# Performance work log

Measured on AMD Instinct MI355X. Metric: run time of the kernel, lower is better.

The kernel has to match this reference:

```python
import jax, jax.numpy as jnp
import numpy as np

DIM = 1024
HEAD_SIZE = 128
B, N = 4, 4096

def setup_inputs() -> dict:
    key = jax.random.key(0)
    kx, kq, kk, kv = jax.random.split(key, 4)
    s = (1.0 / DIM) ** 0.5  # ~ torch Linear init scale
    return {
        "x": jax.random.normal(kx, (B, N, DIM), dtype=jnp.float32),
        "Wq": jax.random.uniform(kq, (HEAD_SIZE, DIM), dtype=jnp.float32, minval=-s, maxval=s),
        "Wk": jax.random.uniform(kk, (HEAD_SIZE, DIM), dtype=jnp.float32, minval=-s, maxval=s),
        "Wv": jax.random.uniform(kv, (HEAD_SIZE, DIM), dtype=jnp.float32, minval=-s, maxval=s),
    }

def reference(x, Wq, Wk, Wv):
    # x: [B, N, dim]; W*: [head_size, dim] (torch Linear convention y = x @ W.T)
    q = jnp.einsum('bnd,hd->bnh', x, Wq)
    k = jnp.einsum('bnd,hd->bnh', x, Wk)
    v = jnp.einsum('bnd,hd->bnh', x, Wv)
    scale = DIM ** (-0.5)  # NOTE: original scales by dim**-0.5, not head_size
    scores = jnp.einsum('bnh,bmh->bnm', q, k) * scale  # [B, N, N]
    weights = jax.nn.softmax(scores, axis=-1)
    context = jnp.einsum('bnm,bmh->bnh', weights, v)  # [B, N, head_size]
    return context
```

## Files before the change

kernel.cpp:

```cpp
#include <hip/hip_runtime.h>

using bf16x8   = __attribute__((ext_vector_type(8))) __bf16;
using f32x4    = __attribute__((ext_vector_type(4))) float;
using f32x16   = __attribute__((ext_vector_type(16))) float;
using floatv4  = __attribute__((ext_vector_type(4))) float;
using ushortv4 = __attribute__((ext_vector_type(4))) unsigned short;
using ushortv8 = __attribute__((ext_vector_type(8))) unsigned short;
using uintv2   = __attribute__((ext_vector_type(2))) unsigned int;
using uintv4   = __attribute__((ext_vector_type(4))) unsigned int;

#define N_SEQ 4096
#define N_B   4
#define DIMK  1024
#define HS    128
#define ROWS  (N_B * N_SEQ)
#define KVB   32
#define TT    (N_SEQ / KVB)
#define CEXPF 0.045084220027780106f

__device__ __forceinline__ unsigned short f2bf(float f) {
    unsigned u = __builtin_bit_cast(unsigned, f);
    u += 0x7FFFu + ((u >> 16) & 1u);
    return (unsigned short)(u >> 16);
}

__device__ __forceinline__ unsigned cvtpk(float lo, float hi) {
    unsigned r;
    asm("v_cvt_pk_bf16_f32 %0, %1, %2" : "=v"(r) : "v"(lo), "v"(hi));
    return r;
}

__device__ __forceinline__ void gload16(const unsigned short* g, unsigned short* l) {
    __builtin_amdgcn_global_load_lds(
        (const __attribute__((address_space(1))) unsigned int*)g,
        (__attribute__((address_space(3))) unsigned int*)l, 16, 0, 0);
}

__global__ __launch_bounds__(256) void castw_kernel(
    const float* __restrict__ Wq,
    const float* __restrict__ Wk,
    const float* __restrict__ Wv,
    unsigned short* __restrict__ Wb2)
{
    const int blk = blockIdx.x;
    const int z = blk >> 6;
    const int b2 = blk & 63;
    const float* src = (z == 0) ? Wq : (z == 1) ? Wk : Wv;
    const float scale = (z == 0) ? CEXPF : 1.0f;

    const int oo = b2 * 256 + threadIdx.x;
    const int slot = oo & 3;
    const int row  = (oo >> 2) & 127;
    const int ks   = oo >> 9;
    const int slog = (slot - (row >> 1)) & 3;
    const int k0   = ks * 32 + slog * 8;

    floatv4 a = *reinterpret_cast<const floatv4*>(src + (size_t)row * DIMK + k0);
    floatv4 b = *reinterpret_cast<const floatv4*>(src + (size_t)row * DIMK + k0 + 4);
    ushortv8 o = { f2bf(a.x*scale), f2bf(a.y*scale), f2bf(a.z*scale), f2bf(a.w*scale),
                   f2bf(b.x*scale), f2bf(b.y*scale), f2bf(b.z*scale), f2bf(b.w*scale) };
    unsigned short* dst = Wb2 + (size_t)ks * 12288 + (size_t)z * 4096 + ((row * 4 + slot) * 8);
    *reinterpret_cast<ushortv8*>(dst) = o;
}

__global__ __launch_bounds__(512, 1) void proj_kernel(
    const float* __restrict__ X,
    const unsigned short* __restrict__ Wb2,
    unsigned short* __restrict__ Qb,
    unsigned short* __restrict__ Kb,
    unsigned short* __restrict__ Vt)
{
    const int row0 = blockIdx.x * 64;
    __shared__ unsigned short smem[2 * 64 * 40 + 2 * 384 * 32];
    unsigned short* Xs = smem;
    unsigned short* Ws = smem + 2 * 64 * 40;
    const int tid = threadIdx.x;
    const int wv = tid >> 6, lane = tid & 63;
    const int lr = lane & 15, lg = lane >> 4;

    const int xr_r = tid >> 3, xr_q = tid & 7;
    const float* xgbase = X + (size_t)(row0 + xr_r) * DIMK + xr_q * 4;

    f32x4 acc[4][3] = {};

    auto loadX = [&](floatv4& xr, int ks) {
        xr = *reinterpret_cast<const floatv4*>(xgbase + ks * 32);
    };
    auto writeX = [&](int buf, const floatv4& xr) {
        uintv2 w = { cvtpk(xr.x, xr.y), cvtpk(xr.z, xr.w) };
        *reinterpret_cast<uintv2*>(&Xs[buf * (64 * 40) + xr_r * 40 + xr_q * 4]) = w;
    };
    auto stageW = [&](int buf, int ks) {
        const unsigned short* src = Wb2 + (size_t)ks * 12288;
        unsigned short* dst = Ws + buf * 12288;
        #pragma unroll
        for (int jj = 0; jj < 3; ++jj)
            gload16(src + (size_t)(jj * 512 + wv * 64 + lane) * 8,
                    dst + (jj * 512 + wv * 64) * 8);
    };

    int zni[3], wrow0[3];
    #pragma unroll
    for (int ni = 0; ni < 3; ++ni) {
        int gc0 = wv * 48 + ni * 16;
        zni[ni] = gc0 >> 7;
        wrow0[ni] = gc0 & 127;
    }

    floatv4 xrA, xrB;
    loadX(xrB, 0); stageW(0, 0);
    loadX(xrA, 1); stageW(1, 1);
    asm volatile("s_waitcnt vmcnt(4)" ::: "memory");
    writeX(0, xrB);
    __syncthreads();

#define PROJ_ITER(KS, XN, XM, CUR)                                             \
    {                                                                          \
        const unsigned short* Xc = Xs + (CUR) * (64 * 40);                     \
        const unsigned short* Wc = Ws + (CUR) * 12288;                         \
        bf16x8 af[4]; bf16x8 bfr[3];                                           \
        _Pragma("unroll")                                                      \
        for (int mi = 0; mi < 4; ++mi)                                         \
            af[mi] = *reinterpret_cast<const bf16x8*>(                         \
                &Xc[(mi * 16 + lr) * 40 + lg * 8]);                            \
        _Pragma("unroll")                                                      \
        for (int ni = 0; ni < 3; ++ni) {                                       \
            int wrow = wrow0[ni] + lr;                                         \
            bfr[ni] = *reinterpret_cast<const bf16x8*>(                        \
                &Wc[((zni[ni] * 128 + wrow) * 4 + ((lg + (wrow >> 1)) & 3)) * 8]); \
        }                                                                      \
        _Pragma("unroll")                                                      \
        for (int mi = 0; mi < 4; ++mi)                                         \
            _Pragma("unroll")                                                  \
            for (int ni = 0; ni < 3; ++ni)                                     \
                acc[mi][ni] = __builtin_amdgcn_mfma_f32_16x16x32_bf16(         \
                    af[mi], bfr[ni], acc[mi][ni], 0, 0, 0);                    \
        __syncthreads();                                                       \
        if ((KS) + 2 < 32) { loadX(XM, (KS) + 2); stageW((CUR), (KS) + 2); }   \
        if ((KS) + 1 < 32) {                                                   \
            if ((KS) + 2 < 32)                                                 \
                asm volatile("s_waitcnt vmcnt(4)" ::: "memory");               \
            else                                                               \
                asm volatile("s_waitcnt vmcnt(0)" ::: "memory");               \
            writeX((CUR) ^ 1, XN);                                             \
            __syncthreads();                                                   \
        }                                                                      \
    }

    for (int kss = 0; kss < 32; kss += 2) {
        PROJ_ITER(kss,     xrA, xrB, 0);
        PROJ_ITER(kss + 1, xrB, xrA, 1);
    }
#undef PROJ_ITER

    unsigned short* Cs = smem;
    #pragma unroll
    for (int ni = 0; ni < 3; ++ni) {
        const int z = zni[ni];
        if (z < 2) {
            unsigned short* O = (z == 0) ? Qb : Kb;
            const int col = wrow0[ni] + lr;
            #pragma unroll
            for (int mi = 0; mi < 4; ++mi) {
                int rowb = row0 + mi * 16 + lg * 4;
                #pragma unroll
                for (int r = 0; r < 4; ++r)
                    O[(size_t)(rowb + r) * HS + col] = f2bf(acc[mi][ni][r]);
            }
        } else {
            const int col = wrow0[ni] + lr;
            #pragma unroll
            for (int mi = 0; mi < 4; ++mi)
                #pragma unroll
                for (int r = 0; r < 4; ++r)
                    Cs[(mi * 16 + lg * 4 + r) * 136 + col] = f2bf(acc[mi][ni][r]);
        }
    }
    __syncthreads();
    {
        const int b  = row0 >> 12;
        const int n0 = row0 & (N_SEQ - 1);
        #pragma unroll
        for (int i = 0; i < 2; ++i) {
            int idx = tid + i * 512;
            int d = idx >> 3, c8 = idx & 7;
            ushortv8 v;
            #pragma unroll
            for (int j = 0; j < 8; ++j)
                v[j] = Cs[(c8 * 8 + j) * 136 + d];
            *reinterpret_cast<ushortv8*>(Vt + (size_t)b * HS * N_SEQ + (size_t)d * N_SEQ + n0 + c8 * 8) = v;
        }
    }
}

__global__ __launch_bounds__(256, 3) void attn_kernel(
    const unsigned short* __restrict__ Qb,
    const unsigned short* __restrict__ Kb,
    const unsigned short* __restrict__ Vt,
    unsigned short* __restrict__ part,
    float* __restrict__ plsum,
    int S)
{
    const int qblk  = blockIdx.x;
    const int split = blockIdx.y;
    const int tid = threadIdx.x;
    const int wv = tid >> 6, lane = tid & 63;
    const int l31 = lane & 31, h = lane >> 5;
    const int b    = qblk >> 5;
    const int row0 = (qblk & 31) * 128 + wv * 32;

    __shared__ unsigned short Ks[3][KVB * 128];
    __shared__ unsigned short Vs[3][128 * KVB];

    bf16x8 qf[8];
    {
        const unsigned short* qp = Qb + ((size_t)b * N_SEQ + row0 + l31) * HS + h * 8;
        #pragma unroll
        for (int kk = 0; kk < 8; ++kk)
            qf[kk] = *reinterpret_cast<const bf16x8*>(qp + kk * 16);
    }

    const int base = TT / S, rem = TT % S;
    const int nt = base + (split < rem ? 1 : 0);
    const int kv_begin = (split * base + (split < rem ? split : rem)) * KVB;

    const unsigned short* Kbb = Kb + (size_t)b * N_SEQ * HS;
    const unsigned short* Vbb = Vt + (size_t)b * HS * N_SEQ;

    auto stage = [&](int buf, int kv0) {
        #pragma unroll
        for (int i = 0; i < 2; ++i) {
            int g = wv * 2 + i;
            int r = g * 4 + (lane >> 4);
            int sp = (lane & 15) ^ (r & 7);
            gload16(Kbb + (size_t)(kv0 + r) * HS + sp * 8, &Ks[buf][g * 4 * 128]);
        }
        #pragma unroll
        for (int i = 0; i < 2; ++i) {
            int g = wv * 2 + i;
            int r = g * 16 + (lane >> 2);
            int sp = (lane & 3) ^ ((r >> 1) & 3);
            gload16(Vbb + (size_t)r * N_SEQ + kv0 + sp * 8, &Vs[buf][g * 16 * KVB]);
        }
    };

    f32x16 ctx[4] = {};
    float lsum = 0.f;

    stage(0, kv_begin);
    stage(1, kv_begin + KVB);
    int cur = 0, nxt = 2;
    for (int t = 0; t < nt; ++t) {
        if (t + 2 < nt) {
            asm volatile("s_waitcnt vmcnt(4)\n\ts_barrier" ::: "memory");
            stage(nxt, kv_begin + (t + 2) * KVB);
        } else if (t + 1 < nt) {
            asm volatile("s_waitcnt vmcnt(4)\n\ts_barrier" ::: "memory");
        } else {
            asm volatile("s_waitcnt vmcnt(0)\n\ts_barrier" ::: "memory");
        }

        f32x16 st0 = {}, st1 = {};
        __builtin_amdgcn_s_setprio(1);
        #pragma unroll
        for (int kk = 0; kk < 8; kk += 2) {
            bf16x8 kf0 = *reinterpret_cast<const bf16x8*>(
                &Ks[cur][l31 * 128 + (((kk * 2 + h) ^ (l31 & 7)) * 8)]);
            st0 = __builtin_amdgcn_mfma_f32_32x32x16_bf16(kf0, qf[kk], st0, 0, 0, 0);
            bf16x8 kf1 = *reinterpret_cast<const bf16x8*>(
                &Ks[cur][l31 * 128 + ((((kk + 1) * 2 + h) ^ (l31 & 7)) * 8)]);
            st1 = __builtin_amdgcn_mfma_f32_32x32x16_bf16(kf1, qf[kk + 1], st1, 0, 0, 0);
        }
        __builtin_amdgcn_s_setprio(0);

        float p[16];
        #pragma unroll
        for (int r = 0; r < 16; ++r)
            p[r] = __builtin_amdgcn_exp2f(st0[r] + st1[r]);

        {
            float a0 = (p[0] + p[1])   + (p[2] + p[3]);
            float a1 = (p[4] + p[5])   + (p[6] + p[7]);
            float a2 = (p[8] + p[9])   + (p[10] + p[11]);
            float a3 = (p[12] + p[13]) + (p[14] + p[15]);
            lsum += (a0 + a1) + (a2 + a3);
        }

        bf16x8 pf[2];
        #pragma unroll
        for (int half = 0; half < 2; ++half) {
            unsigned a  = cvtpk(p[half*8 + 0], p[half*8 + 1]);
            unsigned bq = cvtpk(p[half*8 + 2], p[half*8 + 3]);
            unsigned c  = cvtpk(p[half*8 + 4], p[half*8 + 5]);
            unsigned d  = cvtpk(p[half*8 + 6], p[half*8 + 7]);
            asm("v_permlane32_swap_b32 %0, %1" : "+v"(a), "+v"(c));
            asm("v_permlane32_swap_b32 %0, %1" : "+v"(bq), "+v"(d));
            uintv4 w = { a, bq, c, d };
            pf[half] = __builtin_bit_cast(bf16x8, w);
        }

        __builtin_amdgcn_s_setprio(1);
        #pragma unroll
        for (int dt = 0; dt < 4; ++dt) {
            int d = dt * 32 + l31;
            bf16x8 vf0 = *reinterpret_cast<const bf16x8*>(
                &Vs[cur][d * KVB + (((0 + h) ^ ((d >> 1) & 3)) * 8)]);
            ctx[dt] = __builtin_amdgcn_mfma_f32_32x32x16_bf16(pf[0], vf0, ctx[dt], 0, 0, 0);
            bf16x8 vf1 = *reinterpret_cast<const bf16x8*>(
                &Vs[cur][d * KVB + (((2 + h) ^ ((d >> 1) & 3)) * 8)]);
            ctx[dt] = __builtin_amdgcn_mfma_f32_32x32x16_bf16(pf[1], vf1, ctx[dt], 0, 0, 0);
        }
        __builtin_amdgcn_s_setprio(0);

        cur = (cur == 2) ? 0 : cur + 1;
        nxt = (nxt == 2) ? 0 : nxt + 1;
    }

    lsum += __shfl_xor(lsum, 32);

    const int qt = qblk * 4 + wv;
    unsigned short* pp = part + ((size_t)qt * S + split) * (32 * 128);
    #pragma unroll
    for (int rp = 0; rp < 4; ++rp)
        #pragma unroll
        for (int rq = 0; rq < 4; ++rq) {
            const int r = rp * 4 + rq;
            const int q = rq + 8 * rp + 4 * h;
            #pragma unroll
            for (int dt = 0; dt < 4; ++dt)
                pp[q * 128 + dt * 32 + l31] = (unsigned short)(cvtpk(ctx[dt][r], ctx[dt][r]) & 0xFFFFu);
        }
    if (h == 0)
        plsum[((size_t)qt * S + split) * 32 + l31] = lsum;
}

__global__ __launch_bounds__(256) void reduce_kernel(
    const unsigned short* __restrict__ part,
    const float* __restrict__ plsum,
    float* __restrict__ out, int S)
{
    const int id = blockIdx.x * 256 + threadIdx.x;
    const int d4 = (id & 31) * 4;
    const int grow = id >> 5;
    const int qt = grow >> 5, q = grow & 31;
    f32x4 c = {0.f, 0.f, 0.f, 0.f};
    float l = 0.f;
    for (int s = 0; s < S; ++s) {
        ushortv4 pv = *reinterpret_cast<const ushortv4*>(
            &part[(((size_t)qt * S + s) * 32 + q) * 128 + d4]);
        #pragma unroll
        for (int j = 0; j < 4; ++j)
            c[j] += __builtin_bit_cast(float, (unsigned)pv[j] << 16);
        l += plsum[((size_t)qt * S + s) * 32 + q];
    }
    float inv = 1.0f / l;
    f32x4 o = { c[0]*inv, c[1]*inv, c[2]*inv, c[3]*inv };
    *reinterpret_cast<f32x4*>(&out[(size_t)grow * 128 + d4]) = o;
}

extern "C" void kernel_launch(void* const* d_in, const int* in_sizes, int n_in,
                              void* d_out, int out_size, void* d_ws, size_t ws_size,
                              hipStream_t stream) {
    const float* x  = (const float*)d_in[0];
    const float* wq = (const float*)d_in[1];
    const float* wk = (const float*)d_in[2];
    const float* wv = (const float*)d_in[3];

    unsigned short* Wb2 = (unsigned short*)d_ws;
    unsigned short* Qb = Wb2 + (size_t)3 * HS * DIMK;
    unsigned short* Kb = Qb + (size_t)ROWS * HS;
    unsigned short* Vt = Kb + (size_t)ROWS * HS;
    float* plsum = (float*)(Vt + (size_t)N_B * HS * N_SEQ);

    const size_t fixed = (size_t)3 * HS * DIMK * 2 + (size_t)3 * ROWS * HS * 2;
    const size_t per_split = (size_t)512 * 32 * 4 + (size_t)512 * 32 * 128 * 2;

    int S;
    if      (ws_size >= fixed + 6 * per_split) S = 6;
    else if (ws_size >= fixed + 4 * per_split) S = 4;
    else if (ws_size >= fixed + 2 * per_split) S = 2;
    else                                       S = 1;

    unsigned short* part = (unsigned short*)(plsum + (size_t)512 * S * 32);

    castw_kernel<<<192, 256, 0, stream>>>(wq, wk, wv, Wb2);
    proj_kernel<<<256, 512, 0, stream>>>(x, Wb2, Qb, Kb, Vt);
    attn_kernel<<<dim3(128, S), 256, 0, stream>>>(Qb, Kb, Vt, part, plsum, S);
    reduce_kernel<<<(ROWS * HS) / 1024, 256, 0, stream>>>(part, plsum, (float*)d_out, S);
}
```

Measured before the change: 88.00 us.

## Shrink projection tiles to 32 rows and remap attention blocks across XCDs

The projection kernel moves from 64-row tiles with 512 threads to 32-row tiles with 256 threads, two blocks per CU and 512 blocks. It uses a simpler single-stage prefetch loop and an XOR-swizzled X tile in shared memory in place of padding. The attention launch is flattened to 1D, and for S=6 the block index is remapped so blocks sharing a batch's K/V land on the same XCD, aiming for better L2 reuse. The smaller tiles lower per-block register use and raise occupancy, but each block reloads the full weight tile, doubling weight traffic, and the pipeline now drains with vmcnt(0) every step.

```diff
diff --git a/kernel.cpp b/kernel.cpp
--- a/kernel.cpp
+++ b/kernel.cpp
@@ -63,114 +63,108 @@
     *reinterpret_cast<ushortv8*>(dst) = o;
 }
 
-__global__ __launch_bounds__(512, 1) void proj_kernel(
+__global__ __launch_bounds__(256, 2) void proj_kernel(
     const float* __restrict__ X,
     const unsigned short* __restrict__ Wb2,
     unsigned short* __restrict__ Qb,
     unsigned short* __restrict__ Kb,
     unsigned short* __restrict__ Vt)
 {
-    const int row0 = blockIdx.x * 64;
-    __shared__ unsigned short smem[2 * 64 * 40 + 2 * 384 * 32];
-    unsigned short* Xs = smem;
-    unsigned short* Ws = smem + 2 * 64 * 40;
+    const int row0 = blockIdx.x * 32;
+    __shared__ unsigned short smem[2 * 32 * 32 + 2 * 12288];
+    unsigned short* Xs0 = smem;
+    unsigned short* Ws0 = smem + 2 * 32 * 32;
     const int tid = threadIdx.x;
     const int wv = tid >> 6, lane = tid & 63;
     const int lr = lane & 15, lg = lane >> 4;
 
-    const int xr_r = tid >> 3, xr_q = tid & 7;
-    const float* xgbase = X + (size_t)(row0 + xr_r) * DIMK + xr_q * 4;
-
-    f32x4 acc[4][3] = {};
-
-    auto loadX = [&](floatv4& xr, int ks) {
-        xr = *reinterpret_cast<const floatv4*>(xgbase + ks * 32);
+    const int xrow = tid >> 3, xq = tid & 7;
+    const float* xg = X + (size_t)(row0 + xrow) * DIMK + xq * 4;
+    const int xws = xrow * 32 + (((xq >> 1) ^ ((xrow >> 1) & 3)) * 8) + (xq & 1) * 4;
+    floatv4 xr;
+
+    f32x4 acc[2][6] = {};
+
+    auto loadX = [&](int ks) {
+        xr = *reinterpret_cast<const floatv4*>(xg + ks * 32);
     };
-    auto writeX = [&](int buf, const floatv4& xr) {
+    auto writeX = [&](int buf) {
         uintv2 w = { cvtpk(xr.x, xr.y), cvtpk(xr.z, xr.w) };
-        *reinterpret_cast<uintv2*>(&Xs[buf * (64 * 40) + xr_r * 40 + xr_q * 4]) = w;
+        *reinterpret_cast<uintv2*>(&Xs0[buf * (32 * 32) + xws]) = w;
     };
     auto stageW = [&](int buf, int ks) {
         const unsigned short* src = Wb2 + (size_t)ks * 12288;
-        unsigned short* dst = Ws + buf * 12288;
-        #pragma unroll
-        for (int jj = 0; jj < 3; ++jj)
-            gload16(src + (size_t)(jj * 512 + wv * 64 + lane) * 8,
-                    dst + (jj * 512 + wv * 64) * 8);
+        unsigned short* dst = Ws0 + buf * 12288;
+        #pragma unroll
+        for (int i = 0; i < 6; ++i) {
+            int u = (wv * 6 + i) * 64;
+            gload16(src + (size_t)(u + lane) * 8, dst + u * 8);
+        }
     };
 
-    int zni[3], wrow0[3];
+    int zni[6], wrow0[6];
     #pragma unroll
-    for (int ni = 0; ni < 3; ++ni) {
-        int gc0 = wv * 48 + ni * 16;
+    for (int ni = 0; ni < 6; ++ni) {
+        int gc0 = wv * 96 + ni * 16;
         zni[ni] = gc0 >> 7;
         wrow0[ni] = gc0 & 127;
     }
 
-    floatv4 xrA, xrB;
-    loadX(xrB, 0); stageW(0, 0);
-    loadX(xrA, 1); stageW(1, 1);
-    asm volatile("s_waitcnt vmcnt(4)" ::: "memory");
-    writeX(0, xrB);
+    loadX(0);
+    stageW(0, 0);
+    asm volatile("s_waitcnt vmcnt(0)" ::: "memory");
+    writeX(0);
     __syncthreads();
 
-#define PROJ_ITER(KS, XN, XM, CUR)                                             \
-    {                                                                          \
-        const unsigned short* Xc = Xs + (CUR) * (64 * 40);                     \
-        const unsigned short* Wc = Ws + (CUR) * 12288;                         \
-        bf16x8 af[4]; bf16x8 bfr[3];                                           \
-        _Pragma("unroll")                                                      \
-        for (int mi = 0; mi < 4; ++mi)                                         \
-            af[mi] = *reinterpret_cast<const bf16x8*>(                         \
-                &Xc[(mi * 16 + lr) * 40 + lg * 8]);                            \
-        _Pragma("unroll")                                                      \
-        for (int ni = 0; ni < 3; ++ni) {                                       \
-            int wrow = wrow0[ni] + lr;                                         \
-            bfr[ni] = *reinterpret_cast<const bf16x8*>(                        \
-                &Wc[((zni[ni] * 128 + wrow) * 4 + ((lg + (wrow >> 1)) & 3)) * 8]); \
-        }                                                                      \
-        _Pragma("unroll")                                                      \
-        for (int mi = 0; mi < 4; ++mi)                                         \
-            _Pragma("unroll")                                                  \
-            for (int ni = 0; ni < 3; ++ni)                                     \
-                acc[mi][ni] = __builtin_amdgcn_mfma_f32_16x16x32_bf16(         \
-                    af[mi], bfr[ni], acc[mi][ni], 0, 0, 0);                    \
-        __syncthreads();                                                       \
-        if ((KS) + 2 < 32) { loadX(XM, (KS) + 2); stageW((CUR), (KS) + 2); }   \
-        if ((KS) + 1 < 32) {                                                   \
-            if ((KS) + 2 < 32)                                                 \
-                asm volatile("s_waitcnt vmcnt(4)" ::: "memory");               \
-            else                                                               \
-                asm volatile("s_waitcnt vmcnt(0)" ::: "memory");               \
-            writeX((CUR) ^ 1, XN);                                             \
-            __syncthreads();                                                   \
-        }                                                                      \
-    }
-
-    for (int kss = 0; kss < 32; kss += 2) {
-        PROJ_ITER(kss,     xrA, xrB, 0);
-        PROJ_ITER(kss + 1, xrB, xrA, 1);
-    }
-#undef PROJ_ITER
+    for (int ks = 0; ks < 32; ++ks) {
+        const int cur = ks & 1;
+        const bool more = (ks + 1 < 32);
+        if (more) { loadX(ks + 1); stageW(cur ^ 1, ks + 1); }
+
+        const unsigned short* Xc = Xs0 + cur * (32 * 32);
+        const unsigned short* Wc = Ws0 + cur * 12288;
+        bf16x8 af[2], bfr[6];
+        #pragma unroll
+        for (int mi = 0; mi < 2; ++mi)
+            af[mi] = *reinterpret_cast<const bf16x8*>(
+                &Xc[(mi * 16 + lr) * 32 + ((lg ^ ((lr >> 1) & 3)) * 8)]);
+        #pragma unroll
+        for (int ni = 0; ni < 6; ++ni) {
+            int wrow = wrow0[ni] + lr;
+            bfr[ni] = *reinterpret_cast<const bf16x8*>(
+                &Wc[((zni[ni] * 128 + wrow) * 4 + ((lg + (wrow >> 1)) & 3)) * 8]);
+        }
+        #pragma unroll
+        for (int mi = 0; mi < 2; ++mi)
+            #pragma unroll
+            for (int ni = 0; ni < 6; ++ni)
+                acc[mi][ni] = __builtin_amdgcn_mfma_f32_16x16x32_bf16(
+                    af[mi], bfr[ni], acc[mi][ni], 0, 0, 0);
+
+        if (more) {
+            asm volatile("s_waitcnt vmcnt(0)" ::: "memory");
+            writeX(cur ^ 1);
+        }
+        __syncthreads();
+    }
 
     unsigned short* Cs = smem;
     #pragma unroll
-    for (int ni = 0; ni < 3; ++ni) {
+    for (int ni = 0; ni < 6; ++ni) {
         const int z = zni[ni];
+        const int col = wrow0[ni] + lr;
         if (z < 2) {
             unsigned short* O = (z == 0) ? Qb : Kb;
-            const int col = wrow0[ni] + lr;
-            #pragma unroll
-            for (int mi = 0; mi < 4; ++mi) {
+            #pragma unroll
+            for (int mi = 0; mi < 2; ++mi) {
                 int rowb = row0 + mi * 16 + lg * 4;
                 #pragma unroll
                 for (int r = 0; r < 4; ++r)
                     O[(size_t)(rowb + r) * HS + col] = f2bf(acc[mi][ni][r]);
             }
         } else {
-            const int col = wrow0[ni] + lr;
-            #pragma unroll
-            for (int mi = 0; mi < 4; ++mi)
+            #pragma unroll
+            for (int mi = 0; mi < 2; ++mi)
                 #pragma unroll
                 for (int r = 0; r < 4; ++r)
                     Cs[(mi * 16 + lg * 4 + r) * 136 + col] = f2bf(acc[mi][ni][r]);
@@ -182,8 +176,8 @@
         const int n0 = row0 & (N_SEQ - 1);
         #pragma unroll
         for (int i = 0; i < 2; ++i) {
-            int idx = tid + i * 512;
-            int d = idx >> 3, c8 = idx & 7;
+            int idx = tid + i * 256;
+            int d = idx >> 2, c8 = idx & 3;
             ushortv8 v;
             #pragma unroll
             for (int j = 0; j < 8; ++j)
@@ -201,8 +195,21 @@
     float* __restrict__ plsum,
     int S)
 {
-    const int qblk  = blockIdx.x;
-    const int split = blockIdx.y;
+    int qblk, split;
+    {
+        const int bid = blockIdx.x;
+        if (S == 6) {
+            const int chunk = bid >> 8, r2 = bid & 255;
+            const int member = r2 >> 3, xcd = r2 & 7;
+            const int g = chunk * 8 + xcd;
+            const int bb = g / 6;
+            split = g - bb * 6;
+            qblk = bb * 32 + member;
+        } else {
+            qblk = bid & 127;
+            split = bid >> 7;
+        }
+    }
     const int tid = threadIdx.x;
     const int wv = tid >> 6, lane = tid & 63;
     const int l31 = lane & 31, h = lane >> 5;
@@ -384,7 +391,7 @@
     unsigned short* part = (unsigned short*)(plsum + (size_t)512 * S * 32);
 
     castw_kernel<<<192, 256, 0, stream>>>(wq, wk, wv, Wb2);
-    proj_kernel<<<256, 512, 0, stream>>>(x, Wb2, Qb, Kb, Vt);
-    attn_kernel<<<dim3(128, S), 256, 0, stream>>>(Qb, Kb, Vt, part, plsum, S);
+    proj_kernel<<<512, 256, 0, stream>>>(x, Wb2, Qb, Kb, Vt);
+    attn_kernel<<<dim3(128 * S), 256, 0, stream>>>(Qb, Kb, Vt, part, plsum, S);
     reduce_kernel<<<(ROWS * HS) / 1024, 256, 0, stream>>>(part, plsum, (float*)d_out, S);
 }
```

Measured after the change: 86.52 us. No clear change (-1.7%).
